# Kernel optimization log

Measured on AMD Instinct MI355X. Metric: run time of the kernel, lower is better.

Reference implementation:

```python
import jax, jax.numpy as jnp
import numpy as np
from jax import lax

B, T, C, H, W = 8, 2048, 128, 256, 16
LN_EPS = 1e-5


def setup_inputs() -> dict:
    key = jax.random.key(0)
    ks = jax.random.split(key, 8)
    s_ih = 1.0 / np.sqrt(H)
    return {
        "x": jax.random.normal(ks[0], (B, T, C), jnp.float32),
        "w_ih": jax.random.uniform(ks[1], (3 * H, C), jnp.float32, -s_ih, s_ih),
        "w_hh": jax.random.uniform(ks[2], (3 * H, H), jnp.float32, -s_ih, s_ih),
        "b_ih": jax.random.uniform(ks[3], (3 * H,), jnp.float32, -s_ih, s_ih),
        "b_hh": jax.random.uniform(ks[4], (3 * H,), jnp.float32, -s_ih, s_ih),
        "w_proj": jax.random.normal(ks[5], (H, H), jnp.float32) * (1.0 / np.sqrt(H)),
        "b_proj": jnp.zeros((H,), jnp.float32),
        "ln_gamma": jnp.ones((H,), jnp.float32),
        "ln_beta": jnp.zeros((H,), jnp.float32),
    }


def _sliding_gru(x, w_ih, w_hh, b_ih, b_hh):
    # x: [B,T,C]. Equivalent to running a GRU over each length-W left-padded
    # window ending at t, for all t, returning the final hidden state [B,T,H].
    pad = W - 1
    x_pad = jnp.pad(x, ((0, 0), (pad, 0), (0, 0)))  # [B, T+W-1, C]
    # Precompute input projection once (avoids the [B,T,W,C] unfold buffer).
    xi = jnp.einsum("btc,gc->btg", x_pad, w_ih) + b_ih  # [B, T+W-1, 3H]

    def step(h, w):
        # window step w sees x_pad[:, w : w+T, :] -> precomputed gates slice
        gi = lax.dynamic_slice_in_dim(xi, w, T, axis=1)  # [B,T,3H]
        gh = jnp.einsum("bth,gh->btg", h, w_hh) + b_hh   # [B,T,3H]
        gi_r, gi_z, gi_n = jnp.split(gi, 3, axis=-1)
        gh_r, gh_z, gh_n = jnp.split(gh, 3, axis=-1)
        r = jax.nn.sigmoid(gi_r + gh_r)
        z = jax.nn.sigmoid(gi_z + gh_z)
        n = jnp.tanh(gi_n + r * gh_n)
        h_new = (1.0 - z) * n + z * h
        return h_new, None

    h0 = jnp.zeros((B, T, H), x.dtype)
    h_final, _ = lax.scan(step, h0, jnp.arange(W))
    return h_final  # [B,T,H]


def reference(x, w_ih, w_hh, b_ih, b_hh, w_proj, b_proj, ln_gamma, ln_beta):
    feats = _sliding_gru(x, w_ih, w_hh, b_ih, b_hh)  # [B,T,H]
    y = jnp.einsum("bth,oh->bto", feats, w_proj) + b_proj
    mu = jnp.mean(y, axis=-1, keepdims=True)
    var = jnp.mean(jnp.square(y - mu), axis=-1, keepdims=True)
    y = (y - mu) * lax.rsqrt(var + LN_EPS) * ln_gamma + ln_beta
    return jax.nn.gelu(y, approximate=False)  # dropout is identity in eval
```

## Files before the change

kernel.cpp:

```cpp
#include <hip/hip_runtime.h>
#include <math.h>

typedef unsigned short u16;
typedef unsigned int   u32;
typedef __attribute__((ext_vector_type(8)))  short short8;
typedef __attribute__((ext_vector_type(16))) float f32x16;

#define NT 2048
#define NC 128
#define NH 256
#define NW 16

#define WS_NEEDED 720896

__device__ __forceinline__ u16 f2bf(float f) {
  u32 u = __builtin_bit_cast(u32, f);
  u = u + 0x7fffu + ((u >> 16) & 1u);
  return (u16)(u >> 16);
}
__device__ __forceinline__ float bf2f(u16 v) {
  return __builtin_bit_cast(float, (u32)v << 16);
}
__device__ __forceinline__ float nclamp(float v) {
  return fminf(fmaxf(v, -30.0f), 30.0f);
}
__device__ __forceinline__ float fsig(float x) {
  return __builtin_amdgcn_rcpf(1.0f + __builtin_amdgcn_exp2f(-1.44269504f * x));
}
__device__ __forceinline__ float ftanhf(float x) {
  float e = __builtin_amdgcn_exp2f(2.88539008f * x);
  return 1.0f - 2.0f * __builtin_amdgcn_rcpf(e + 1.0f);
}
__device__ __forceinline__ float gelu(float v) {
  return 0.5f * v * (1.0f + erff(v * 0.70710678118654752f));
}

__global__ void pack_w(const float* __restrict__ whh, const float* __restrict__ wih,
                       const float* __restrict__ wpr,
                       u16* __restrict__ whh_p, u16* __restrict__ wih_p,
                       u16* __restrict__ wpr_p) {
  int t = blockIdx.x * 256 + threadIdx.x;
  u16 v[8];
  if (t < 24576) {
    int lane = t & 63, kit = (t >> 6) & 15, nt = t >> 10;
    int wv = nt / 3, g = nt - wv * 3;
    int grow = g * 256 + wv * 32 + (lane & 31);
    int kb = kit * 16 + (lane >> 5) * 8;
    #pragma unroll
    for (int e = 0; e < 8; ++e) v[e] = f2bf(whh[grow * 256 + kb + e]);
    u32* d = (u32*)(whh_p + (size_t)t * 8);
    #pragma unroll
    for (int e = 0; e < 4; ++e) d[e] = (u32)v[2*e] | ((u32)v[2*e+1] << 16);
  } else if (t < 36864) {
    int t2 = t - 24576;
    int lane = t2 & 63, kit = (t2 >> 6) & 7, nt = t2 >> 9;
    int wv = nt / 3, g = nt - wv * 3;
    int grow = g * 256 + wv * 32 + (lane & 31);
    int kb = kit * 16 + (lane >> 5) * 8;
    #pragma unroll
    for (int e = 0; e < 8; ++e) v[e] = f2bf(wih[grow * 128 + kb + e]);
    u32* d = (u32*)(wih_p + (size_t)t2 * 8);
    #pragma unroll
    for (int e = 0; e < 4; ++e) d[e] = (u32)v[2*e] | ((u32)v[2*e+1] << 16);
  } else if (t < 45056) {
    int t3 = t - 36864;
    int lane = t3 & 63, kit = (t3 >> 6) & 15, nt = t3 >> 10;
    int o = nt * 32 + (lane & 31);
    int kb = kit * 16 + (lane >> 5) * 8;
    #pragma unroll
    for (int e = 0; e < 8; ++e) v[e] = f2bf(wpr[o * 256 + kb + e]);
    u32* d = (u32*)(wpr_p + (size_t)t3 * 8);
    #pragma unroll
    for (int e = 0; e < 4; ++e) d[e] = (u32)v[2*e] | ((u32)v[2*e+1] << 16);
  }
}

__device__ __forceinline__ short8 cvt8(const float* p) {
  float4 a = *(const float4*)p, b = *(const float4*)(p + 4);
  u16 v0 = f2bf(a.x), v1 = f2bf(a.y), v2 = f2bf(a.z), v3 = f2bf(a.w);
  u16 v4 = f2bf(b.x), v5 = f2bf(b.y), v6 = f2bf(b.z), v7 = f2bf(b.w);
  u32 r0 = (u32)v0 | ((u32)v1 << 16), r1 = (u32)v2 | ((u32)v3 << 16);
  u32 r2 = (u32)v4 | ((u32)v5 << 16), r3 = (u32)v6 | ((u32)v7 << 16);
  uint4 r = make_uint4(r0, r1, r2, r3);
  return __builtin_bit_cast(short8, r);
}

template<int USEWS>
__global__ __launch_bounds__(512, 2) void gru_mfma(
    const float* __restrict__ x, const float* __restrict__ b_ih, const float* __restrict__ b_hh,
    const float* __restrict__ wih, const float* __restrict__ whh, const float* __restrict__ wpr,
    const u16* __restrict__ wih_p, const u16* __restrict__ whh_p, const u16* __restrict__ wpr_p,
    const float* __restrict__ c256_0, const float* __restrict__ c256_1, const float* __restrict__ c256_2,
    float* __restrict__ out) {
  __shared__ u16 xs[80 * 128];
  __shared__ u16 hb[2][64 * 256];
  const int tid = threadIdx.x, wv = tid >> 6, lane = tid & 63;
  const int ml = lane & 31, lh = lane >> 5;
  const int wg = blockIdx.x;
  const int bidx = wg >> 5, t0 = (wg & 31) * 64;
  const long R0 = (long)wg * 64;
  const int j = wv * 32 + ml;

  const float *gp, *bpp, *bep;
  {
    float v0 = c256_0[0], v1 = c256_1[0];
    if (fabsf(v0 - 1.0f) < 0.25f)      { gp = c256_0; bpp = c256_1; bep = c256_2; }
    else if (fabsf(v1 - 1.0f) < 0.25f) { gp = c256_1; bpp = c256_0; bep = c256_2; }
    else                               { gp = c256_2; bpp = c256_0; bep = c256_1; }
  }

  const float br  = b_ih[j]          + b_hh[j];
  const float bz  = b_ih[NH + j]     + b_hh[NH + j];
  const float bni = b_ih[2 * NH + j];
  const float bnh = b_hh[2 * NH + j];

  {
    int r = tid >> 3, c0e = (tid & 7) * 16;
    #pragma unroll
    for (int pass = 0; pass < 2; ++pass) {
      int rr = r + pass * 64;
      if (rr < 79) {
        int tx = t0 + rr - (NW - 1);
        float vv[16];
        if (tx >= 0) {
          const float4* src = (const float4*)(x + ((long)bidx * NT + tx) * NC + c0e);
          #pragma unroll
          for (int q = 0; q < 4; ++q) {
            float4 f = src[q];
            vv[q*4+0] = f.x; vv[q*4+1] = f.y; vv[q*4+2] = f.z; vv[q*4+3] = f.w;
          }
        } else {
          #pragma unroll
          for (int q = 0; q < 16; ++q) vv[q] = 0.0f;
        }
        int byb = rr * 256 + c0e * 2;
        int sw = (rr & 15) << 4;
        #pragma unroll
        for (int ch = 0; ch < 2; ++ch) {
          u32 q0 = (u32)f2bf(vv[ch*8+0]) | ((u32)f2bf(vv[ch*8+1]) << 16);
          u32 q1 = (u32)f2bf(vv[ch*8+2]) | ((u32)f2bf(vv[ch*8+3]) << 16);
          u32 q2 = (u32)f2bf(vv[ch*8+4]) | ((u32)f2bf(vv[ch*8+5]) << 16);
          u32 q3 = (u32)f2bf(vv[ch*8+6]) | ((u32)f2bf(vv[ch*8+7]) << 16);
          *(uint4*)((char*)xs + ((byb + ch * 16) ^ sw)) = make_uint4(q0, q1, q2, q3);
        }
      }
    }
  }
  __syncthreads();

  float hreg[2][16];
  #pragma unroll
  for (int mt = 0; mt < 2; ++mt)
    #pragma unroll
    for (int rg = 0; rg < 16; ++rg) hreg[mt][rg] = 0.0f;

  const int swh = (ml & 15) << 4;

  for (int s = 0; s < NW; ++s) {
    f32x16 acc[2][4];
    #pragma unroll
    for (int mt = 0; mt < 2; ++mt)
      #pragma unroll
      for (int g = 0; g < 4; ++g)
        #pragma unroll
        for (int e = 0; e < 16; ++e) acc[mt][g][e] = 0.0f;

    if (s > 0) {
      const u16* hc = hb[(s + 1) & 1];
      #pragma unroll 4
      for (int kit = 0; kit < 16; ++kit) {
        short8 a0 = *(const short8*)((const char*)hc +
                      ((ml * 512 + kit * 32 + lh * 16) ^ swh));
        short8 a1 = *(const short8*)((const char*)hc +
                      (((ml + 32) * 512 + kit * 32 + lh * 16) ^ swh));
        #pragma unroll
        for (int g = 0; g < 3; ++g) {
          short8 bfr;
          if (USEWS)
            bfr = __builtin_bit_cast(short8,
                    ((const uint4*)whh_p)[(((wv * 3 + g) * 16) + kit) * 64 + lane]);
          else
            bfr = cvt8(whh + (g * 256 + wv * 32 + ml) * 256 + kit * 16 + lh * 8);
          const int ga = (g == 2) ? 3 : g;
          acc[0][ga] = __builtin_amdgcn_mfma_f32_32x32x16_bf16(a0, bfr, acc[0][ga], 0, 0, 0);
          acc[1][ga] = __builtin_amdgcn_mfma_f32_32x32x16_bf16(a1, bfr, acc[1][ga], 0, 0, 0);
        }
      }
    }

    {
      int r0 = s + ml;
      int sw0 = (r0 & 15) << 4;
      #pragma unroll 4
      for (int kit = 0; kit < 8; ++kit) {
        short8 a0 = *(const short8*)((const char*)xs +
                      ((r0 * 256 + kit * 32 + lh * 16) ^ sw0));
        short8 a1 = *(const short8*)((const char*)xs +
                      (((r0 + 32) * 256 + kit * 32 + lh * 16) ^ sw0));
        #pragma unroll
        for (int g = 0; g < 3; ++g) {
          short8 bfr;
          if (USEWS)
            bfr = __builtin_bit_cast(short8,
                    ((const uint4*)wih_p)[((wv * 3 + g) * 8 + kit) * 64 + lane]);
          else
            bfr = cvt8(wih + (g * 256 + wv * 32 + ml) * 128 + kit * 16 + lh * 8);
          acc[0][g] = __builtin_amdgcn_mfma_f32_32x32x16_bf16(a0, bfr, acc[0][g], 0, 0, 0);
          acc[1][g] = __builtin_amdgcn_mfma_f32_32x32x16_bf16(a1, bfr, acc[1][g], 0, 0, 0);
        }
      }
    }

    u16* hn = hb[s & 1];
    #pragma unroll
    for (int mt = 0; mt < 2; ++mt) {
      #pragma unroll
      for (int rg = 0; rg < 16; ++rg) {
        int m = mt * 32 + (rg & 3) + 8 * (rg >> 2) + 4 * lh;
        float r = fsig(nclamp(acc[mt][0][rg] + br));
        float z = fsig(nclamp(acc[mt][1][rg] + bz));
        float n = ftanhf(nclamp(acc[mt][2][rg] + bni + r * (acc[mt][3][rg] + bnh)));
        float hv = n + z * (hreg[mt][rg] - n);
        hreg[mt][rg] = hv;
        *(u16*)((char*)hn + ((m * 512 + j * 2) ^ ((m & 15) << 4))) = f2bf(hv);
      }
    }
    __syncthreads();
  }

  f32x16 pc[2];
  #pragma unroll
  for (int mt = 0; mt < 2; ++mt)
    #pragma unroll
    for (int e = 0; e < 16; ++e) pc[mt][e] = 0.0f;
  const u16* hf = hb[1];
  #pragma unroll 4
  for (int kit = 0; kit < 16; ++kit) {
    short8 a0 = *(const short8*)((const char*)hf +
                  ((ml * 512 + kit * 32 + lh * 16) ^ swh));
    short8 a1 = *(const short8*)((const char*)hf +
                  (((ml + 32) * 512 + kit * 32 + lh * 16) ^ swh));
    short8 bfr;
    if (USEWS)
      bfr = __builtin_bit_cast(short8, ((const uint4*)wpr_p)[(wv * 16 + kit) * 64 + lane]);
    else
      bfr = cvt8(wpr + (wv * 32 + ml) * 256 + kit * 16 + lh * 8);
    pc[0] = __builtin_amdgcn_mfma_f32_32x32x16_bf16(a0, bfr, pc[0], 0, 0, 0);
    pc[1] = __builtin_amdgcn_mfma_f32_32x32x16_bf16(a1, bfr, pc[1], 0, 0, 0);
  }
  const float bp = bpp[j];
  #pragma unroll
  for (int mt = 0; mt < 2; ++mt) {
    #pragma unroll
    for (int rg = 0; rg < 16; ++rg) {
      int m = mt * 32 + (rg & 3) + 8 * (rg >> 2) + 4 * lh;
      *(u16*)((char*)hb[0] + ((m * 512 + j * 2) ^ ((m & 15) << 4))) = f2bf(pc[mt][rg] + bp);
    }
  }
  __syncthreads();

  {
    int m = tid >> 3, cg = (tid & 7) * 32;
    int sw = (m & 15) << 4;
    float v[32];
    #pragma unroll
    for (int q = 0; q < 4; ++q) {
      uint4 raw = *(const uint4*)((char*)hb[0] + ((m * 512 + cg * 2 + q * 16) ^ sw));
      u32 w4[4] = {raw.x, raw.y, raw.z, raw.w};
      #pragma unroll
      for (int e = 0; e < 4; ++e) {
        v[q * 8 + e * 2]     = bf2f((u16)(w4[e] & 0xffffu));
        v[q * 8 + e * 2 + 1] = bf2f((u16)(w4[e] >> 16));
      }
    }
    float s1 = 0.0f, s2 = 0.0f;
    #pragma unroll
    for (int i = 0; i < 32; ++i) { s1 += v[i]; s2 += v[i] * v[i]; }
    #pragma unroll
    for (int d = 1; d < 8; d <<= 1) {
      s1 += __shfl_xor(s1, d, 64);
      s2 += __shfl_xor(s2, d, 64);
    }
    float mu = s1 * (1.0f / 256.0f);
    float var = s2 * (1.0f / 256.0f) - mu * mu;
    if (!(var > 0.0f)) var = 0.0f;
    float rstd = rsqrtf(var + 1e-5f);
    float* od = out + (R0 + m) * NH + cg;
    #pragma unroll
    for (int q = 0; q < 8; ++q) {
      int i0 = q * 4;
      float o0 = gelu((v[i0]     - mu) * rstd * gp[cg + i0]     + bep[cg + i0]);
      float o1 = gelu((v[i0 + 1] - mu) * rstd * gp[cg + i0 + 1] + bep[cg + i0 + 1]);
      float o2 = gelu((v[i0 + 2] - mu) * rstd * gp[cg + i0 + 2] + bep[cg + i0 + 2]);
      float o3 = gelu((v[i0 + 3] - mu) * rstd * gp[cg + i0 + 3] + bep[cg + i0 + 3]);
      *(float4*)(od + i0) = make_float4(o0, o1, o2, o3);
    }
  }
}

extern "C" void kernel_launch(void* const* d_in, const int* in_sizes, int n_in,
                              void* d_out, int out_size, void* d_ws, size_t ws_size,
                              hipStream_t stream) {
  (void)out_size;
  const float *x = nullptr, *wih = nullptr, *whh = nullptr, *b768a = nullptr,
              *b768b = nullptr, *wpr = nullptr, *c0 = nullptr, *c1 = nullptr,
              *c2 = nullptr;
  int n768 = 0, n256 = 0;
  for (int i = 0; i < n_in; ++i) {
    const float* p = (const float*)d_in[i];
    switch (in_sizes[i]) {
      case 2097152: x = p; break;
      case 98304:   wih = p; break;
      case 196608:  whh = p; break;
      case 65536:   wpr = p; break;
      case 768:     { if (n768 == 0) b768a = p; else b768b = p; ++n768; } break;
      case 256:     { if (n256 == 0) c0 = p; else if (n256 == 1) c1 = p; else c2 = p; ++n256; } break;
      default: break;
    }
  }
  char* ws = (char*)d_ws;
  u16* whh_p = (u16*)(ws + 0);
  u16* wih_p = (u16*)(ws + 393216);
  u16* wpr_p = (u16*)(ws + 589824);
  float* outp = (float*)d_out;

  if (ws_size >= (size_t)WS_NEEDED) {
    pack_w<<<dim3(176), dim3(256), 0, stream>>>(whh, wih, wpr, whh_p, wih_p, wpr_p);
    gru_mfma<1><<<dim3(256), dim3(512), 0, stream>>>(x, b768a, b768b, wih, whh, wpr,
                                                     wih_p, whh_p, wpr_p,
                                                     c0, c1, c2, outp);
  } else {
    gru_mfma<0><<<dim3(256), dim3(512), 0, stream>>>(x, b768a, b768b, wih, whh, wpr,
                                                     nullptr, nullptr, nullptr,
                                                     c0, c1, c2, outp);
  }
}
```

Before: 217.0 us.

## Precompute input gate projection once in a separate kernel instead of per window step

Adds xi_kernel, which computes the x·W_ih projection plus bias for every padded time step once and stores it as bf16 in workspace. The main GRU kernel then reads these precomputed gates per step rather than redoing the input MFMA 16 times per tile, which removes about a third of the recurrent matmul work. It also drops the double-buffered h in LDS in favour of a single buffer with an extra barrier, and remaps block indices across batches. The cost is a larger workspace, an extra launch, strided global gate reads on every step, and bf16 rounding of the input gates.

```diff
diff --git a/kernel.cpp b/kernel.cpp
--- a/kernel.cpp
+++ b/kernel.cpp
@@ -10,8 +10,10 @@
 #define NC 128
 #define NH 256
 #define NW 16
-
-#define WS_NEEDED 720896
+#define TPAD 2063
+
+#define WS_GI_OFF 720896
+#define WS_NEEDED (WS_GI_OFF + (size_t)8 * TPAD * 256 * 8)
 
 __device__ __forceinline__ u16 f2bf(float f) {
   u32 u = __builtin_bit_cast(u32, f);
@@ -20,6 +22,12 @@
 }
 __device__ __forceinline__ float bf2f(u16 v) {
   return __builtin_bit_cast(float, (u32)v << 16);
+}
+__device__ __forceinline__ float bflo(u32 w) {
+  return __builtin_bit_cast(float, w << 16);
+}
+__device__ __forceinline__ float bfhi(u32 w) {
+  return __builtin_bit_cast(float, w & 0xffff0000u);
 }
 __device__ __forceinline__ float nclamp(float v) {
   return fminf(fmaxf(v, -30.0f), 30.0f);
@@ -75,6 +83,240 @@
   }
 }
 
+__global__ __launch_bounds__(512, 2) void xi_kernel(
+    const float* __restrict__ x, const float* __restrict__ b_ih,
+    const u16* __restrict__ wih_p, uint2* __restrict__ gi) {
+  __shared__ u16 xs[64 * 128];
+  const int tid = threadIdx.x, wv = tid >> 6, lane = tid & 63;
+  const int ml = lane & 31, lh = lane >> 5;
+  const int b = blockIdx.x / 33, chunk = blockIdx.x % 33;
+  const int tp0 = chunk * 64;
+  const int j = wv * 32 + ml;
+
+  {
+    int r = tid >> 3, c0e = (tid & 7) * 16;
+    int xr = tp0 + r - (NW - 1);
+    float vv[16];
+    if (xr >= 0 && xr < NT) {
+      const float4* src = (const float4*)(x + ((long)b * NT + xr) * NC + c0e);
+      #pragma unroll
+      for (int q = 0; q < 4; ++q) {
+        float4 f = src[q];
+        vv[q*4+0] = f.x; vv[q*4+1] = f.y; vv[q*4+2] = f.z; vv[q*4+3] = f.w;
+      }
+    } else {
+      #pragma unroll
+      for (int q = 0; q < 16; ++q) vv[q] = 0.0f;
+    }
+    int byb = r * 256 + c0e * 2;
+    int sw = (r & 15) << 4;
+    #pragma unroll
+    for (int ch = 0; ch < 2; ++ch) {
+      u32 q0 = (u32)f2bf(vv[ch*8+0]) | ((u32)f2bf(vv[ch*8+1]) << 16);
+      u32 q1 = (u32)f2bf(vv[ch*8+2]) | ((u32)f2bf(vv[ch*8+3]) << 16);
+      u32 q2 = (u32)f2bf(vv[ch*8+4]) | ((u32)f2bf(vv[ch*8+5]) << 16);
+      u32 q3 = (u32)f2bf(vv[ch*8+6]) | ((u32)f2bf(vv[ch*8+7]) << 16);
+      *(uint4*)((char*)xs + ((byb + ch * 16) ^ sw)) = make_uint4(q0, q1, q2, q3);
+    }
+  }
+  __syncthreads();
+
+  const float bi0 = b_ih[j], bi1 = b_ih[NH + j], bi2 = b_ih[2 * NH + j];
+  f32x16 acc[2][3];
+  #pragma unroll
+  for (int mt = 0; mt < 2; ++mt) {
+    #pragma unroll
+    for (int e = 0; e < 16; ++e) {
+      acc[mt][0][e] = bi0; acc[mt][1][e] = bi1; acc[mt][2][e] = bi2;
+    }
+  }
+
+  const int sw0 = (ml & 15) << 4;
+  #pragma unroll 4
+  for (int kit = 0; kit < 8; ++kit) {
+    short8 a0 = *(const short8*)((const char*)xs +
+                  ((ml * 256 + kit * 32 + lh * 16) ^ sw0));
+    short8 a1 = *(const short8*)((const char*)xs +
+                  (((ml + 32) * 256 + kit * 32 + lh * 16) ^ sw0));
+    #pragma unroll
+    for (int g = 0; g < 3; ++g) {
+      short8 bfr = __builtin_bit_cast(short8,
+                     ((const uint4*)wih_p)[((wv * 3 + g) * 8 + kit) * 64 + lane]);
+      acc[0][g] = __builtin_amdgcn_mfma_f32_32x32x16_bf16(a0, bfr, acc[0][g], 0, 0, 0);
+      acc[1][g] = __builtin_amdgcn_mfma_f32_32x32x16_bf16(a1, bfr, acc[1][g], 0, 0, 0);
+    }
+  }
+
+  #pragma unroll
+  for (int mt = 0; mt < 2; ++mt) {
+    #pragma unroll
+    for (int rg = 0; rg < 16; ++rg) {
+      int m = mt * 32 + (rg & 3) + 8 * (rg >> 2) + 4 * lh;
+      int tp = tp0 + m;
+      if (tp < TPAD) {
+        u32 rz = (u32)f2bf(acc[mt][0][rg]) | ((u32)f2bf(acc[mt][1][rg]) << 16);
+        u32 nn = (u32)f2bf(acc[mt][2][rg]);
+        gi[((long)b * TPAD + tp) * 256 + j] = make_uint2(rz, nn);
+      }
+    }
+  }
+}
+
+__global__ __launch_bounds__(512, 2) void gru_main(
+    const float* __restrict__ b_hh,
+    const u16* __restrict__ whh_p, const u16* __restrict__ wpr_p,
+    const uint2* __restrict__ gi,
+    const float* __restrict__ c256_0, const float* __restrict__ c256_1,
+    const float* __restrict__ c256_2, float* __restrict__ out) {
+  __shared__ u16 hbuf[64 * 256];
+  const int tid = threadIdx.x, wv = tid >> 6, lane = tid & 63;
+  const int ml = lane & 31, lh = lane >> 5;
+  const int wg = (blockIdx.x & 7) * 32 + (blockIdx.x >> 3);
+  const int bidx = wg >> 5, t0 = (wg & 31) * 64;
+  const long R0 = (long)wg * 64;
+  const int j = wv * 32 + ml;
+
+  const float *gp, *bpp, *bep;
+  {
+    float v0 = c256_0[0], v1 = c256_1[0];
+    if (fabsf(v0 - 1.0f) < 0.25f)      { gp = c256_0; bpp = c256_1; bep = c256_2; }
+    else if (fabsf(v1 - 1.0f) < 0.25f) { gp = c256_1; bpp = c256_0; bep = c256_2; }
+    else                               { gp = c256_2; bpp = c256_0; bep = c256_1; }
+  }
+
+  const float bhr = b_hh[j], bhz = b_hh[NH + j], bnh = b_hh[2 * NH + j];
+  const uint2* gib = gi + ((long)bidx * TPAD + t0) * 256 + j;
+
+  float hreg[2][16];
+  #pragma unroll
+  for (int mt = 0; mt < 2; ++mt)
+    #pragma unroll
+    for (int rg = 0; rg < 16; ++rg) hreg[mt][rg] = 0.0f;
+
+  const int swh = (ml & 15) << 4;
+
+  for (int s = 0; s < NW; ++s) {
+    u32 grz[2][16], gn[2][16];
+    #pragma unroll
+    for (int mt = 0; mt < 2; ++mt) {
+      #pragma unroll
+      for (int rg = 0; rg < 16; ++rg) {
+        int m = mt * 32 + (rg & 3) + 8 * (rg >> 2) + 4 * lh;
+        uint2 gv = gib[(long)(s + m) * 256];
+        grz[mt][rg] = gv.x; gn[mt][rg] = gv.y;
+      }
+    }
+
+    f32x16 acc[2][3];
+    #pragma unroll
+    for (int mt = 0; mt < 2; ++mt) {
+      #pragma unroll
+      for (int e = 0; e < 16; ++e) {
+        acc[mt][0][e] = bhr; acc[mt][1][e] = bhz; acc[mt][2][e] = bnh;
+      }
+    }
+
+    if (s > 0) {
+      #pragma unroll 4
+      for (int kit = 0; kit < 16; ++kit) {
+        short8 a0 = *(const short8*)((const char*)hbuf +
+                      ((ml * 512 + kit * 32 + lh * 16) ^ swh));
+        short8 a1 = *(const short8*)((const char*)hbuf +
+                      (((ml + 32) * 512 + kit * 32 + lh * 16) ^ swh));
+        #pragma unroll
+        for (int g = 0; g < 3; ++g) {
+          short8 bfr = __builtin_bit_cast(short8,
+                         ((const uint4*)whh_p)[(((wv * 3 + g) * 16) + kit) * 64 + lane]);
+          acc[0][g] = __builtin_amdgcn_mfma_f32_32x32x16_bf16(a0, bfr, acc[0][g], 0, 0, 0);
+          acc[1][g] = __builtin_amdgcn_mfma_f32_32x32x16_bf16(a1, bfr, acc[1][g], 0, 0, 0);
+        }
+      }
+    }
+    __syncthreads();
+
+    #pragma unroll
+    for (int mt = 0; mt < 2; ++mt) {
+      #pragma unroll
+      for (int rg = 0; rg < 16; ++rg) {
+        int m = mt * 32 + (rg & 3) + 8 * (rg >> 2) + 4 * lh;
+        float r = fsig(nclamp(bflo(grz[mt][rg]) + acc[mt][0][rg]));
+        float z = fsig(nclamp(bfhi(grz[mt][rg]) + acc[mt][1][rg]));
+        float n = ftanhf(nclamp(bflo(gn[mt][rg]) + r * acc[mt][2][rg]));
+        float hv = n + z * (hreg[mt][rg] - n);
+        hreg[mt][rg] = hv;
+        *(u16*)((char*)hbuf + ((m * 512 + j * 2) ^ ((m & 15) << 4))) = f2bf(hv);
+      }
+    }
+    __syncthreads();
+  }
+
+  f32x16 pc[2];
+  #pragma unroll
+  for (int mt = 0; mt < 2; ++mt)
+    #pragma unroll
+    for (int e = 0; e < 16; ++e) pc[mt][e] = 0.0f;
+  #pragma unroll 4
+  for (int kit = 0; kit < 16; ++kit) {
+    short8 a0 = *(const short8*)((const char*)hbuf +
+                  ((ml * 512 + kit * 32 + lh * 16) ^ swh));
+    short8 a1 = *(const short8*)((const char*)hbuf +
+                  (((ml + 32) * 512 + kit * 32 + lh * 16) ^ swh));
+    short8 bfr = __builtin_bit_cast(short8,
+                   ((const uint4*)wpr_p)[(wv * 16 + kit) * 64 + lane]);
+    pc[0] = __builtin_amdgcn_mfma_f32_32x32x16_bf16(a0, bfr, pc[0], 0, 0, 0);
+    pc[1] = __builtin_amdgcn_mfma_f32_32x32x16_bf16(a1, bfr, pc[1], 0, 0, 0);
+  }
+  const float bp = bpp[j];
+  __syncthreads();
+  #pragma unroll
+  for (int mt = 0; mt < 2; ++mt) {
+    #pragma unroll
+    for (int rg = 0; rg < 16; ++rg) {
+      int m = mt * 32 + (rg & 3) + 8 * (rg >> 2) + 4 * lh;
+      *(u16*)((char*)hbuf + ((m * 512 + j * 2) ^ ((m & 15) << 4))) = f2bf(pc[mt][rg] + bp);
+    }
+  }
+  __syncthreads();
+
+  {
+    int m = tid >> 3, cg = (tid & 7) * 32;
+    int sw = (m & 15) << 4;
+    float v[32];
+    #pragma unroll
+    for (int q = 0; q < 4; ++q) {
+      uint4 raw = *(const uint4*)((char*)hbuf + ((m * 512 + cg * 2 + q * 16) ^ sw));
+      u32 w4[4] = {raw.x, raw.y, raw.z, raw.w};
+      #pragma unroll
+      for (int e = 0; e < 4; ++e) {
+        v[q * 8 + e * 2]     = bflo(w4[e]);
+        v[q * 8 + e * 2 + 1] = bfhi(w4[e]);
+      }
+    }
+    float s1 = 0.0f, s2 = 0.0f;
+    #pragma unroll
+    for (int i = 0; i < 32; ++i) { s1 += v[i]; s2 += v[i] * v[i]; }
+    #pragma unroll
+    for (int d = 1; d < 8; d <<= 1) {
+      s1 += __shfl_xor(s1, d, 64);
+      s2 += __shfl_xor(s2, d, 64);
+    }
+    float mu = s1 * (1.0f / 256.0f);
+    float var = s2 * (1.0f / 256.0f) - mu * mu;
+    if (!(var > 0.0f)) var = 0.0f;
+    float rstd = rsqrtf(var + 1e-5f);
+    float* od = out + (R0 + m) * NH + cg;
+    #pragma unroll
+    for (int q = 0; q < 8; ++q) {
+      int i0 = q * 4;
+      float o0 = gelu((v[i0]     - mu) * rstd * gp[cg + i0]     + bep[cg + i0]);
+      float o1 = gelu((v[i0 + 1] - mu) * rstd * gp[cg + i0 + 1] + bep[cg + i0 + 1]);
+      float o2 = gelu((v[i0 + 2] - mu) * rstd * gp[cg + i0 + 2] + bep[cg + i0 + 2]);
+      float o3 = gelu((v[i0 + 3] - mu) * rstd * gp[cg + i0 + 3] + bep[cg + i0 + 3]);
+      *(float4*)(od + i0) = make_float4(o0, o1, o2, o3);
+    }
+  }
+}
+
 __device__ __forceinline__ short8 cvt8(const float* p) {
   float4 a = *(const float4*)p, b = *(const float4*)(p + 4);
   u16 v0 = f2bf(a.x), v1 = f2bf(a.y), v2 = f2bf(a.z), v3 = f2bf(a.w);
@@ -85,13 +327,11 @@
   return __builtin_bit_cast(short8, r);
 }
 
-template<int USEWS>
-__global__ __launch_bounds__(512, 2) void gru_mfma(
+__global__ __launch_bounds__(512, 2) void gru_fb(
     const float* __restrict__ x, const float* __restrict__ b_ih, const float* __restrict__ b_hh,
     const float* __restrict__ wih, const float* __restrict__ whh, const float* __restrict__ wpr,
-    const u16* __restrict__ wih_p, const u16* __restrict__ whh_p, const u16* __restrict__ wpr_p,
-    const float* __restrict__ c256_0, const float* __restrict__ c256_1, const float* __restrict__ c256_2,
-    float* __restrict__ out) {
+    const float* __restrict__ c256_0, const float* __restrict__ c256_1,
+    const float* __restrict__ c256_2, float* __restrict__ out) {
   __shared__ u16 xs[80 * 128];
   __shared__ u16 hb[2][64 * 256];
   const int tid = threadIdx.x, wv = tid >> 6, lane = tid & 63;
@@ -100,7 +340,6 @@
   const int bidx = wg >> 5, t0 = (wg & 31) * 64;
   const long R0 = (long)wg * 64;
   const int j = wv * 32 + ml;
-
   const float *gp, *bpp, *bep;
   {
     float v0 = c256_0[0], v1 = c256_1[0];
@@ -108,12 +347,10 @@
     else if (fabsf(v1 - 1.0f) < 0.25f) { gp = c256_1; bpp = c256_0; bep = c256_2; }
     else                               { gp = c256_2; bpp = c256_0; bep = c256_1; }
   }
-
-  const float br  = b_ih[j]          + b_hh[j];
-  const float bz  = b_ih[NH + j]     + b_hh[NH + j];
+  const float br  = b_ih[j] + b_hh[j];
+  const float bz  = b_ih[NH + j] + b_hh[NH + j];
   const float bni = b_ih[2 * NH + j];
   const float bnh = b_hh[2 * NH + j];
-
   {
     int r = tid >> 3, c0e = (tid & 7) * 16;
     #pragma unroll
@@ -147,15 +384,12 @@
     }
   }
   __syncthreads();
-
   float hreg[2][16];
   #pragma unroll
   for (int mt = 0; mt < 2; ++mt)
     #pragma unroll
     for (int rg = 0; rg < 16; ++rg) hreg[mt][rg] = 0.0f;
-
   const int swh = (ml & 15) << 4;
-
   for (int s = 0; s < NW; ++s) {
     f32x16 acc[2][4];
     #pragma unroll
@@ -164,7 +398,6 @@
       for (int g = 0; g < 4; ++g)
         #pragma unroll
         for (int e = 0; e < 16; ++e) acc[mt][g][e] = 0.0f;
-
     if (s > 0) {
       const u16* hc = hb[(s + 1) & 1];
       #pragma unroll 4
@@ -175,19 +408,13 @@
                       (((ml + 32) * 512 + kit * 32 + lh * 16) ^ swh));
         #pragma unroll
         for (int g = 0; g < 3; ++g) {
-          short8 bfr;
-          if (USEWS)
-            bfr = __builtin_bit_cast(short8,
-                    ((const uint4*)whh_p)[(((wv * 3 + g) * 16) + kit) * 64 + lane]);
-          else
-            bfr = cvt8(whh + (g * 256 + wv * 32 + ml) * 256 + kit * 16 + lh * 8);
+          short8 bfr = cvt8(whh + (g * 256 + wv * 32 + ml) * 256 + kit * 16 + lh * 8);
           const int ga = (g == 2) ? 3 : g;
           acc[0][ga] = __builtin_amdgcn_mfma_f32_32x32x16_bf16(a0, bfr, acc[0][ga], 0, 0, 0);
           acc[1][ga] = __builtin_amdgcn_mfma_f32_32x32x16_bf16(a1, bfr, acc[1][ga], 0, 0, 0);
         }
       }
     }
-
     {
       int r0 = s + ml;
       int sw0 = (r0 & 15) << 4;
@@ -199,18 +426,12 @@
                       (((r0 + 32) * 256 + kit * 32 + lh * 16) ^ sw0));
         #pragma unroll
         for (int g = 0; g < 3; ++g) {
-          short8 bfr;
-          if (USEWS)
-            bfr = __builtin_bit_cast(short8,
-                    ((const uint4*)wih_p)[((wv * 3 + g) * 8 + kit) * 64 + lane]);
-          else
-            bfr = cvt8(wih + (g * 256 + wv * 32 + ml) * 128 + kit * 16 + lh * 8);
+          short8 bfr = cvt8(wih + (g * 256 + wv * 32 + ml) * 128 + kit * 16 + lh * 8);
           acc[0][g] = __builtin_amdgcn_mfma_f32_32x32x16_bf16(a0, bfr, acc[0][g], 0, 0, 0);
           acc[1][g] = __builtin_amdgcn_mfma_f32_32x32x16_bf16(a1, bfr, acc[1][g], 0, 0, 0);
         }
       }
     }
-
     u16* hn = hb[s & 1];
     #pragma unroll
     for (int mt = 0; mt < 2; ++mt) {
@@ -227,7 +448,6 @@
     }
     __syncthreads();
   }
-
   f32x16 pc[2];
   #pragma unroll
   for (int mt = 0; mt < 2; ++mt)
@@ -240,11 +460,7 @@
                   ((ml * 512 + kit * 32 + lh * 16) ^ swh));
     short8 a1 = *(const short8*)((const char*)hf +
                   (((ml + 32) * 512 + kit * 32 + lh * 16) ^ swh));
-    short8 bfr;
-    if (USEWS)
-      bfr = __builtin_bit_cast(short8, ((const uint4*)wpr_p)[(wv * 16 + kit) * 64 + lane]);
-    else
-      bfr = cvt8(wpr + (wv * 32 + ml) * 256 + kit * 16 + lh * 8);
+    short8 bfr = cvt8(wpr + (wv * 32 + ml) * 256 + kit * 16 + lh * 8);
     pc[0] = __builtin_amdgcn_mfma_f32_32x32x16_bf16(a0, bfr, pc[0], 0, 0, 0);
     pc[1] = __builtin_amdgcn_mfma_f32_32x32x16_bf16(a1, bfr, pc[1], 0, 0, 0);
   }
@@ -258,7 +474,6 @@
     }
   }
   __syncthreads();
-
   {
     int m = tid >> 3, cg = (tid & 7) * 32;
     int sw = (m & 15) << 4;
@@ -269,8 +484,8 @@
       u32 w4[4] = {raw.x, raw.y, raw.z, raw.w};
       #pragma unroll
       for (int e = 0; e < 4; ++e) {
-        v[q * 8 + e * 2]     = bf2f((u16)(w4[e] & 0xffffu));
-        v[q * 8 + e * 2 + 1] = bf2f((u16)(w4[e] >> 16));
+        v[q * 8 + e * 2]     = bflo(w4[e]);
+        v[q * 8 + e * 2 + 1] = bfhi(w4[e]);
       }
     }
     float s1 = 0.0f, s2 = 0.0f;
@@ -322,16 +537,16 @@
   u16* whh_p = (u16*)(ws + 0);
   u16* wih_p = (u16*)(ws + 393216);
   u16* wpr_p = (u16*)(ws + 589824);
+  uint2* gi  = (uint2*)(ws + WS_GI_OFF);
   float* outp = (float*)d_out;
 
-  if (ws_size >= (size_t)WS_NEEDED) {
+  if (ws_size >= WS_NEEDED) {
     pack_w<<<dim3(176), dim3(256), 0, stream>>>(whh, wih, wpr, whh_p, wih_p, wpr_p);
-    gru_mfma<1><<<dim3(256), dim3(512), 0, stream>>>(x, b768a, b768b, wih, whh, wpr,
-                                                     wih_p, whh_p, wpr_p,
-                                                     c0, c1, c2, outp);
+    xi_kernel<<<dim3(264), dim3(512), 0, stream>>>(x, b768a, wih_p, gi);
+    gru_main<<<dim3(256), dim3(512), 0, stream>>>(b768b, whh_p, wpr_p, gi,
+                                                  c0, c1, c2, outp);
   } else {
-    gru_mfma<0><<<dim3(256), dim3(512), 0, stream>>>(x, b768a, b768b, wih, whh, wpr,
-                                                     nullptr, nullptr, nullptr,
-                                                     c0, c1, c2, outp);
-  }
-}
+    gru_fb<<<dim3(256), dim3(512), 0, stream>>>(x, b768a, b768b, wih, whh, wpr,
+                                                c0, c1, c2, outp);
+  }
+}
```

After: 328.7 us. +51.5%, slower.
